# Kernel tuning notes

Measured on AMD Instinct MI355X. Metric: run time of the kernel, lower is better.

## Reference

```python
import jax, jax.numpy as jnp
import numpy as np

_NORM12 = np.array([[3,1,1,1,3,3,3,3],[1,3,1,1,3,3,3,3],[1,1,3,1,3,3,3,3],[1,1,1,3,3,3,3,3],[3,3,3,1,3,3,1,1],[3,3,3,1,3,1,3,1],[3,3,3,1,1,3,3,1],[3,3,3,1,3,1,1,3],[3,3,3,1,1,3,1,3],[3,3,3,1,1,1,3,3],[3,3,1,3,3,3,1,1],[3,3,1,3,3,1,3,1],[3,3,1,3,1,3,3,1],[3,3,1,3,3,1,1,3],[3,3,1,3,1,3,1,3],[3,3,1,3,1,1,3,3],[3,1,3,3,3,3,1,1],[3,1,3,3,3,1,3,1],[3,1,3,3,1,3,3,1],[3,1,3,3,3,1,1,3],[3,1,3,3,1,3,1,3],[1,3,3,3,1,1,3,3],[1,3,3,3,3,3,1,1],[1,3,3,3,3,1,3,1],[1,3,3,3,1,3,3,1],[1,3,3,3,3,1,1,3],[1,3,3,3,1,3,1,3],[1,1,3,3,1,3,3,3],[3,3,1,1,3,3,3,1]], dtype=np.float32) / 2.0


def _build_tables():
    # abs_grid: nonneg half-integer D8+1/2 abs patterns with norm^2 <= 10 (227 rows,
    # lexicographically sorted like torch.unique(dim=0)), plus 29 norm-12 extras -> 256 rows.
    vals = np.arange(4, dtype=np.float32) + 0.5  # {0.5,1.5,2.5,3.5}
    mesh = np.stack(np.meshgrid(*([vals] * 8), indexing='ij'), axis=-1).reshape(-1, 8)
    d8abs = mesh[(mesh ** 2).sum(-1) <= 10.0]
    d8abs = np.unique(d8abs, axis=0)
    abs_grid = np.concatenate([d8abs, _NORM12], axis=0)  # [256, 8]
    grid_abs_odd = (np.round(abs_grid.sum(-1)).astype(np.int64) % 2) == 1
    # grid_part = E8 lattice points (even # of sign flips of abs rows, last coord
    # pre-negated for odd-sum rows) filtered to: at most one of the first 7 coords < 0
    # and min(first 7) >= -0.5. This equals _E8P_GRID[_PARITY_IDX] + 0.25 after filtering.
    ap = abs_grid.copy()
    ap[:, 7] *= np.where(grid_abs_odd, -1.0, 1.0).astype(np.float32)
    bits = (np.arange(256)[:, None] >> np.arange(8)[None, :]) & 1
    signs = (1.0 - 2.0 * bits[(bits.sum(-1) % 2) == 0]).astype(np.float32)  # [128, 8]
    pts = (ap[:, None, :] * signs[None, :, :]).reshape(-1, 8)
    keep = ((pts[:, :7] < 0).sum(-1) <= 1) & (pts[:, :7].min(-1) >= -0.5)
    grid_part = pts[keep]
    grid_part_norm = (grid_part ** 2).sum(-1)
    # part_abs_map: nearest abs_grid row of |grid_part| (exact match; same argmax form as torch)
    scores = 2.0 * np.abs(grid_part) @ abs_grid.T - (abs_grid ** 2).sum(-1)
    part_abs_map = scores.argmax(-1).astype(np.int32)
    return grid_part, grid_part_norm, part_abs_map, grid_abs_odd


def setup_inputs() -> dict:
    gp, gpn, pam, gao = _build_tables()
    key = jax.random.key(0)
    X = jax.random.normal(key, (131072, 8), dtype=jnp.float32)
    return {
        'X': X,
        'grid_part': jnp.asarray(gp, dtype=jnp.float32),
        'grid_part_norm': jnp.asarray(gpn, dtype=jnp.float32),
        'part_abs_map': jnp.asarray(pam, dtype=jnp.int32),
        'grid_abs_odd': jnp.asarray(gao),
        'bit_map': jnp.asarray(2 ** np.arange(8), dtype=jnp.int32),
    }


_PERM = jnp.array([0, 2, 4, 6, 1, 3, 5, 7])


def _fast_quantize_part(X, grid_part, grid_part_norm, part_abs_map, grid_abs_odd, bit_map, parity):
    Xa = jnp.abs(X)
    neg = X < 0
    odd_row = (neg.sum(-1) % 2) == 1                       # [m]
    flip = (jnp.arange(8) == 7)[None, :] & odd_row[:, None]  # negate col 7 for odd rows
    X_part = jnp.where(flip, -Xa, Xa)
    mask = 1.0 - 2.0 * neg.astype(X.dtype)
    mask = jnp.where(flip, -mask, mask)
    scores = 2.0 * (X_part @ grid_part.T) - grid_part_norm  # [m, G]
    Xqidx = jnp.argmax(scores, axis=-1)
    roundout = grid_part[Xqidx]                            # [m, 8]
    vals = roundout * mask
    err = jnp.sqrt(jnp.sum((X - vals) ** 2, axis=-1))
    abs_idx = part_abs_map[Xqidx].astype(jnp.int32)
    sign_mask = ((roundout < 0) ^ (mask < 0))[:, _PERM]
    sign_mask = sign_mask.at[:, 7].set(sign_mask[:, 7] ^ grid_abs_odd[abs_idx])
    sign_mask = sign_mask.at[:, 0].set(sign_mask[:, 0] ^ parity)
    mask_idx = jnp.sum(sign_mask.astype(jnp.int32) * bit_map, axis=-1)
    idx = (abs_idx << 8) + mask_idx
    return vals, idx, err


def reference(X, grid_part, grid_part_norm, part_abs_map, grid_abs_odd, bit_map):
    quarter = jnp.asarray(0.25, X.dtype)
    pv, pi, pe = _fast_quantize_part(X + quarter, grid_part, grid_part_norm, part_abs_map, grid_abs_odd, bit_map, True)
    mv, mi, me = _fast_quantize_part(X - quarter, grid_part, grid_part_norm, part_abs_map, grid_abs_odd, bit_map, False)
    which = pe < me
    final_vals = jnp.where(which[:, None], pv - quarter, mv + quarter)
    final_idx = jnp.where(which, pi, mi)
    return final_vals, final_idx
```

## Files before the change

kernel.cpp:

```cpp
#include <hip/hip_runtime.h>
#include <math.h>

#define NT   256
#define ROWS 128
#define NW   4
#define MAXA 320

typedef _Float16 h8 __attribute__((ext_vector_type(8)));

static __device__ __forceinline__ unsigned f16_ru(float v) {
    _Float16 h = (_Float16)v;
    unsigned short b;
    __builtin_memcpy(&b, &h, 2);
    if ((float)h < v) b = (b & 0x8000) ? (unsigned short)(b - 1) : (unsigned short)(b + 1);
    return (unsigned)b;
}
static __device__ __forceinline__ float f16_lo(unsigned bits) {
    unsigned short s = (unsigned short)(bits & 0xffffu);
    _Float16 h;
    __builtin_memcpy(&h, &s, 2);
    return (float)h;
}

__global__ __launch_bounds__(NT, 4)
void e8p_quant_kernel(const float* __restrict__ X,
                      const float* __restrict__ gp,
                      const float* __restrict__ gn,
                      const int* __restrict__ pam,
                      float* __restrict__ out,
                      int N, int G)
{
#pragma clang fp contract(off)
    __shared__ h8             labs[MAXA];
    __shared__ unsigned short lmeta[MAXA];
    __shared__ unsigned short lj0[MAXA];
    __shared__ float    cb_bb[2][NW][ROWS];
    __shared__ float    cb_ev[2][NW][ROWS];
    __shared__ unsigned cb_h [2][NW][ROWS];
    __shared__ unsigned cb_ij[2][NW][ROWS];

    const int NG = pam[G - 1] + 1;

    const float4* gp4 = reinterpret_cast<const float4*>(gp);
    for (int j = threadIdx.x; j < G; j += NT) {
        int a = pam[j];
        bool st = (j == 0) || (pam[j - 1] != a);
        if (st) {
            float4 A = gp4[2 * j], B = gp4[2 * j + 1];
            float gv[8] = {A.x, A.y, A.z, A.w, B.x, B.y, B.z, B.w};
            h8 h;
#pragma unroll
            for (int k = 0; k < 8; ++k) h[k] = (_Float16)gv[k];
            labs[a] = h;
            int hm = 0;
#pragma unroll
            for (int k = 0; k < 7; ++k) hm |= int(fabsf(gv[k]) == 0.5f) << k;
            int nc = (int)((gn[j] - 2.0f) * 4.0f + 0.5f);
            lmeta[a] = (unsigned short)(hm | (nc << 8));
            lj0[a] = (unsigned short)j;
        }
    }
    __syncthreads();

    const int lane = threadIdx.x & 63;
    const int w    = threadIdx.x >> 6;
    const int rb   = blockIdx.x * ROWS;

    float xf[2][8], xp[2][8], xm[2][8];
    int msbp[2], msbm[2], oddp[2], oddm[2];
    float DLT[2];
    const float4* x4 = reinterpret_cast<const float4*>(X);
#pragma unroll
    for (int rr = 0; rr < 2; ++rr) {
        int r = rb + lane + (rr << 6);
        int rc = (r < N) ? r : (N - 1);
        float4 a0 = x4[2 * rc], a1 = x4[2 * rc + 1];
        float xr[8] = {a0.x, a0.y, a0.z, a0.w, a1.x, a1.y, a1.z, a1.w};
        int nbp = 0, nbm = 0; float Sp = 0.f, Sm = 0.f;
#pragma unroll
        for (int k = 0; k < 8; ++k) {
            xf[rr][k] = xr[k];
            float sp = xr[k] + 0.25f, sm = xr[k] - 0.25f;
            nbp |= int(sp < 0.f) << k;  nbm |= int(sm < 0.f) << k;
            xp[rr][k] = fabsf(sp);  xm[rr][k] = fabsf(sm);
            Sp += xp[rr][k]; Sm += xm[rr][k];
        }
        int op = __popc(nbp) & 1, om = __popc(nbm) & 1;
        if (op) xp[rr][7] = -xp[rr][7];
        if (om) xm[rr][7] = -xm[rr][7];
        oddp[rr] = op; oddm[rr] = om;
        msbp[rr] = nbp ^ (op << 7);  msbm[rr] = nbm ^ (om << 7);
        DLT[rr] = fmaf(3.5f * fmaxf(Sp, Sm), 3.0e-6f, 2.5e-5f);
    }

    float bt[2][2], ev[2][2], s0v[2][2], s1v[2][2];
    int   i0[2][2], i1[2][2];
#pragma unroll
    for (int rr = 0; rr < 2; ++rr)
#pragma unroll
        for (int pp = 0; pp < 2; ++pp) {
            bt[rr][pp] = -3.0e38f; ev[rr][pp] = -3.0e38f;
            s0v[rr][pp] = -3.0e38f; s1v[rr][pp] = -3.0e38f;
            i0[rr][pp] = 0; i1[rr][pp] = 0;
        }

    const int Q = (NG + NW - 1) / NW;
    const int abeg = w * Q, aend = min(NG, abeg + Q);

    for (int a = abeg; a < aend; ++a) {
        h8 hv = labs[a];
        int meta = __builtin_amdgcn_readfirstlane((int)lmeta[a]);
        int hm = meta & 0x7f;
        float nnh = fmaf(-0.125f, (float)(meta >> 8), -1.0f);
        float g0=(float)hv[0], g1=(float)hv[1], g2=(float)hv[2], g3=(float)hv[3];
        float g4=(float)hv[4], g5=(float)hv[5], g6=(float)hv[6], g7=(float)hv[7];
        float m2c7 = -2.0f * g7;

        float sc[2][2], wv[2][2], rm[2][2];
#pragma unroll
        for (int rr = 0; rr < 2; ++rr) {
            float s = fmaf(xp[rr][0], g0, nnh);
            s = fmaf(xp[rr][1], g1, s); s = fmaf(xp[rr][2], g2, s);
            s = fmaf(xp[rr][3], g3, s); s = fmaf(xp[rr][4], g4, s);
            s = fmaf(xp[rr][5], g5, s); s = fmaf(xp[rr][6], g6, s);
            s = fmaf(xp[rr][7], g7, s);
            sc[rr][0] = s;
            float t = fmaf(xm[rr][0], g0, nnh);
            t = fmaf(xm[rr][1], g1, t); t = fmaf(xm[rr][2], g2, t);
            t = fmaf(xm[rr][3], g3, t); t = fmaf(xm[rr][4], g4, t);
            t = fmaf(xm[rr][5], g5, t); t = fmaf(xm[rr][6], g6, t);
            t = fmaf(xm[rr][7], g7, t);
            sc[rr][1] = t;
            wv[rr][0] = fmaf(m2c7, xp[rr][7], s);
            wv[rr][1] = fmaf(m2c7, xm[rr][7], t);
            rm[rr][0] = s; rm[rr][1] = t;
        }
#pragma unroll
        for (int i = 0; i < 7; ++i) {
            if (hm & (1 << i)) {
                rm[0][0] = fmaxf(rm[0][0], wv[0][0] - xp[0][i]);
                rm[0][1] = fmaxf(rm[0][1], wv[0][1] - xm[0][i]);
                rm[1][0] = fmaxf(rm[1][0], wv[1][0] - xp[1][i]);
                rm[1][1] = fmaxf(rm[1][1], wv[1][1] - xm[1][i]);
            }
        }
#pragma unroll
        for (int rr = 0; rr < 2; ++rr)
#pragma unroll
            for (int pp = 0; pp < 2; ++pp) {
                float v = rm[rr][pp];
                if (v >= bt[rr][pp]) {
                    ev[rr][pp] = fmaxf(ev[rr][pp], s1v[rr][pp]);
                    s1v[rr][pp] = s0v[rr][pp]; i1[rr][pp] = i0[rr][pp];
                    s0v[rr][pp] = v;           i0[rr][pp] = a;
                    bt[rr][pp] = fmaxf(bt[rr][pp], v - DLT[rr]);
                }
            }
    }

#pragma unroll
    for (int rr = 0; rr < 2; ++rr) {
        int rowL = lane + (rr << 6);
#pragma unroll
        for (int pp = 0; pp < 2; ++pp) {
            cb_bb[pp][w][rowL] = fmaxf(s0v[rr][pp], fmaxf(s1v[rr][pp], ev[rr][pp]));
            cb_ev[pp][w][rowL] = ev[rr][pp];
            cb_h [pp][w][rowL] = f16_ru(s0v[rr][pp]) | (f16_ru(s1v[rr][pp]) << 16);
            cb_ij[pp][w][rowL] = (unsigned)i0[rr][pp] | ((unsigned)i1[rr][pp] << 16);
        }
    }
    __syncthreads();

    const int t = threadIdx.x;
    if (t >= ROWS) return;
    const int row = rb + t;
    if (row >= N) return;
    const int rs = (t >= 64) ? 1 : 0;

    double xpd[8], xmd[8];
#pragma unroll
    for (int k = 0; k < 8; ++k) {
        double xd = (double)xf[rs][k];
        xpd[k] = fabs(xd + 0.25);
        xmd[k] = fabs(xd - 0.25);
    }
    if (oddp[rs]) xpd[7] = -xpd[7];
    if (oddm[rs]) xmd[7] = -xmd[7];

    auto evalRow = [&](int a, const double* xd, double& bd, int& brow, int& bflip) {
        h8 hv = labs[a];
        int meta = (int)lmeta[a];
        int hm = meta & 0x7f;
        double nd = 2.0 + 0.25 * (double)(meta >> 8);
        double a0=(double)(float)hv[0], a1=(double)(float)hv[1];
        double a2=(double)(float)hv[2], a3=(double)(float)hv[3];
        double a4=(double)(float)hv[4], a5=(double)(float)hv[5];
        double a6=(double)(float)hv[6], a7=(double)(float)hv[7];
        double s = xd[0] * a0;
        s = fma(xd[1], a1, s); s = fma(xd[2], a2, s); s = fma(xd[3], a3, s);
        s = fma(xd[4], a4, s); s = fma(xd[5], a5, s); s = fma(xd[6], a6, s);
        s = fma(xd[7], a7, s);
        double sc0 = fma(2.0, s, -nd);
        if (sc0 > bd) { bd = sc0; brow = a; bflip = -1; }
        double sb2 = sc0 - 4.0 * (xd[7] * a7);
#pragma unroll
        for (int i = 0; i < 7; ++i) {
            if (hm & (1 << i)) {
                double sv = sb2 - 2.0 * xd[i];
                if (sv > bd) { bd = sv; brow = a; bflip = i; }
            }
        }
    };

    auto resolve = [&](int pp, const double* xd, int& browO, int& bflipO) {
        float B = fmaxf(fmaxf(cb_bb[pp][0][t], cb_bb[pp][1][t]),
                        fmaxf(cb_bb[pp][2][t], cb_bb[pp][3][t]));
        float thr = B - DLT[rs];
        bool ok = (cb_ev[pp][0][t] < thr) && (cb_ev[pp][1][t] < thr) &&
                  (cb_ev[pp][2][t] < thr) && (cb_ev[pp][3][t] < thr);
        double bd = -1.0e300; int brow = 0, bflip = -1;
        if (ok) {
#pragma unroll
            for (int w2 = 0; w2 < NW; ++w2) {
                unsigned hh = cb_h[pp][w2][t], ij = cb_ij[pp][w2][t];
                if (f16_lo(hh >> 16) >= thr) evalRow((int)(ij >> 16), xd, bd, brow, bflip);
                if (f16_lo(hh & 0xffffu) >= thr) evalRow((int)(ij & 0xffffu), xd, bd, brow, bflip);
            }
        } else {
            for (int a = 0; a < NG; ++a) evalRow(a, xd, bd, brow, bflip);
        }
        browO = brow; bflipO = bflip;
    };

    int prow, pflip, mrow, mflip;
    resolve(0, xpd, prow, pflip);
    resolve(1, xmd, mrow, mflip);

    double vp[8], vm[8];
    double errP, errM; int idxP, idxM;
    auto finish = [&](int brow, int bflip, double sgn_quarter, int msb, int par,
                      double* v, double& errO, int& idxO) {
#pragma clang fp contract(off)
        h8 hv = labs[brow];
        float g[8];
#pragma unroll
        for (int k = 0; k < 8; ++k) g[k] = (float)hv[k];
        if (bflip >= 0) {
#pragma unroll
            for (int k = 0; k < 7; ++k) if (bflip == k) g[k] = -g[k];
            g[7] = -g[7];
        }
        int gneg = 0; float sumabs = 0.0f;
#pragma unroll
        for (int k = 0; k < 8; ++k) {
            gneg |= int(g[k] < 0.0f) << k;
            sumabs += fabsf(g[k]);
        }
        double vv[8];
#pragma unroll
        for (int k = 0; k < 8; ++k) {
            unsigned u = __float_as_uint(g[k]) ^ ((((unsigned)msb >> k) & 1u) << 31);
            double val = (double)__uint_as_float(u);
            vv[k] = val;
            v[k] = val;
        }
        double d[8];
#pragma unroll
        for (int k = 0; k < 8; ++k) {
            double xs = (double)xf[rs][k] + sgn_quarter;
            d[k] = xs - vv[k];
        }
        double q0 = d[0]*d[0], q1 = d[1]*d[1], q2 = d[2]*d[2], q3 = d[3]*d[3];
        double q4 = d[4]*d[4], q5 = d[5]*d[5], q6 = d[6]*d[6], q7 = d[7]*d[7];
        double e = ((q0 + q1) + (q2 + q3)) + ((q4 + q5) + (q6 + q7));
        errO = sqrt(e);
        int godd = ((int)(sumabs + 0.5f)) & 1;
        int sb = gneg ^ msb;
        int mi = (((sb >> 0) & 1) ^ par)
               | (((sb >> 2) & 1) << 1)
               | (((sb >> 4) & 1) << 2)
               | (((sb >> 6) & 1) << 3)
               | (((sb >> 1) & 1) << 4)
               | (((sb >> 3) & 1) << 5)
               | (((sb >> 5) & 1) << 6)
               | ((((sb >> 7) & 1) ^ godd) << 7);
        idxO = (brow << 8) + mi;
    };

    finish(prow, pflip, +0.25, msbp[rs], 1, vp, errP, idxP);
    finish(mrow, mflip, -0.25, msbm[rs], 0, vm, errM, idxM);
    bool which = errP < errM;

    float ov[8];
#pragma unroll
    for (int k = 0; k < 8; ++k) {
        double o = which ? (vp[k] - 0.25) : (vm[k] + 0.25);
        ov[k] = (float)o;
    }
    float4* o4 = reinterpret_cast<float4*>(out + (size_t)row * 8);
    o4[0] = make_float4(ov[0], ov[1], ov[2], ov[3]);
    o4[1] = make_float4(ov[4], ov[5], ov[6], ov[7]);
    out[(size_t)N * 8 + row] = (float)(which ? idxP : idxM);
}

extern "C" void kernel_launch(void* const* d_in, const int* in_sizes, int n_in,
                              void* d_out, int out_size, void* d_ws, size_t ws_size,
                              hipStream_t stream)
{
    const float* X   = (const float*)d_in[0];
    const float* gp  = (const float*)d_in[1];
    const float* gn  = (const float*)d_in[2];
    const int*   pam = (const int*)d_in[3];
    float* out = (float*)d_out;

    int N = in_sizes[0] / 8;
    int G = in_sizes[1] / 8;
    int blocks = (N + ROWS - 1) / ROWS;
    e8p_quant_kernel<<<blocks, NT, 0, stream>>>(X, gp, gn, pam, out, N, G);
}
```

Measured before the change: 74.62 us.

## Pack plus/minus scores into float2 FMA and branchless top-2 update

The plus- and minus-shift vectors are packed as float2 pairs so the scoring dot products and corrections can map to packed FP32 instructions (v_pk_fma_f32 on CDNA). The per-coordinate max of (wv - x_i) is rewritten as wv minus the min over masked coordinates, which cuts the number of max operations. The top-2 candidate update becomes branchless selects, and the loop is unrolled by 2. An unused shared array is also dropped. The min-based rewrite changes floating-point rounding slightly relative to the per-term max, which could shift near-tie decisions.

New measurement: 99.86 us. 1.34x slower.

```diff
diff --git a/kernel.cpp b/kernel.cpp
--- a/kernel.cpp
+++ b/kernel.cpp
@@ -7,6 +7,7 @@
 #define MAXA 320
 
 typedef _Float16 h8 __attribute__((ext_vector_type(8)));
+typedef float    v2f __attribute__((ext_vector_type(2)));
 
 static __device__ __forceinline__ unsigned f16_ru(float v) {
     _Float16 h = (_Float16)v;
@@ -33,7 +34,6 @@
 #pragma clang fp contract(off)
     __shared__ h8             labs[MAXA];
     __shared__ unsigned short lmeta[MAXA];
-    __shared__ unsigned short lj0[MAXA];
     __shared__ float    cb_bb[2][NW][ROWS];
     __shared__ float    cb_ev[2][NW][ROWS];
     __shared__ unsigned cb_h [2][NW][ROWS];
@@ -57,7 +57,6 @@
             for (int k = 0; k < 7; ++k) hm |= int(fabsf(gv[k]) == 0.5f) << k;
             int nc = (int)((gn[j] - 2.0f) * 4.0f + 0.5f);
             lmeta[a] = (unsigned short)(hm | (nc << 8));
-            lj0[a] = (unsigned short)j;
         }
     }
     __syncthreads();
@@ -66,7 +65,8 @@
     const int w    = threadIdx.x >> 6;
     const int rb   = blockIdx.x * ROWS;
 
-    float xf[2][8], xp[2][8], xm[2][8];
+    float xf[2][8];
+    v2f   xv[2][8];
     int msbp[2], msbm[2], oddp[2], oddm[2];
     float DLT[2];
     const float4* x4 = reinterpret_cast<const float4*>(X);
@@ -77,20 +77,23 @@
         float4 a0 = x4[2 * rc], a1 = x4[2 * rc + 1];
         float xr[8] = {a0.x, a0.y, a0.z, a0.w, a1.x, a1.y, a1.z, a1.w};
         int nbp = 0, nbm = 0; float Sp = 0.f, Sm = 0.f;
+        float xpf[8], xmf[8];
 #pragma unroll
         for (int k = 0; k < 8; ++k) {
             xf[rr][k] = xr[k];
             float sp = xr[k] + 0.25f, sm = xr[k] - 0.25f;
             nbp |= int(sp < 0.f) << k;  nbm |= int(sm < 0.f) << k;
-            xp[rr][k] = fabsf(sp);  xm[rr][k] = fabsf(sm);
-            Sp += xp[rr][k]; Sm += xm[rr][k];
+            xpf[k] = fabsf(sp);  xmf[k] = fabsf(sm);
+            Sp += xpf[k]; Sm += xmf[k];
         }
         int op = __popc(nbp) & 1, om = __popc(nbm) & 1;
-        if (op) xp[rr][7] = -xp[rr][7];
-        if (om) xm[rr][7] = -xm[rr][7];
+        if (op) xpf[7] = -xpf[7];
+        if (om) xmf[7] = -xmf[7];
         oddp[rr] = op; oddm[rr] = om;
         msbp[rr] = nbp ^ (op << 7);  msbm[rr] = nbm ^ (om << 7);
         DLT[rr] = fmaf(3.5f * fmaxf(Sp, Sm), 3.0e-6f, 2.5e-5f);
+#pragma unroll
+        for (int k = 0; k < 8; ++k) xv[rr][k] = (v2f){xpf[k], xmf[k]};
     }
 
     float bt[2][2], ev[2][2], s0v[2][2], s1v[2][2];
@@ -107,6 +110,7 @@
     const int Q = (NG + NW - 1) / NW;
     const int abeg = w * Q, aend = min(NG, abeg + Q);
 
+#pragma unroll 2
     for (int a = abeg; a < aend; ++a) {
         h8 hv = labs[a];
         int meta = __builtin_amdgcn_readfirstlane((int)lmeta[a]);
@@ -115,46 +119,45 @@
         float g0=(float)hv[0], g1=(float)hv[1], g2=(float)hv[2], g3=(float)hv[3];
         float g4=(float)hv[4], g5=(float)hv[5], g6=(float)hv[6], g7=(float)hv[7];
         float m2c7 = -2.0f * g7;
-
-        float sc[2][2], wv[2][2], rm[2][2];
+        v2f nn2 = {nnh, nnh};
+        v2f c72 = {m2c7, m2c7};
+
+        v2f rmv[2];
 #pragma unroll
         for (int rr = 0; rr < 2; ++rr) {
-            float s = fmaf(xp[rr][0], g0, nnh);
-            s = fmaf(xp[rr][1], g1, s); s = fmaf(xp[rr][2], g2, s);
-            s = fmaf(xp[rr][3], g3, s); s = fmaf(xp[rr][4], g4, s);
-            s = fmaf(xp[rr][5], g5, s); s = fmaf(xp[rr][6], g6, s);
-            s = fmaf(xp[rr][7], g7, s);
-            sc[rr][0] = s;
-            float t = fmaf(xm[rr][0], g0, nnh);
-            t = fmaf(xm[rr][1], g1, t); t = fmaf(xm[rr][2], g2, t);
-            t = fmaf(xm[rr][3], g3, t); t = fmaf(xm[rr][4], g4, t);
-            t = fmaf(xm[rr][5], g5, t); t = fmaf(xm[rr][6], g6, t);
-            t = fmaf(xm[rr][7], g7, t);
-            sc[rr][1] = t;
-            wv[rr][0] = fmaf(m2c7, xp[rr][7], s);
-            wv[rr][1] = fmaf(m2c7, xm[rr][7], t);
-            rm[rr][0] = s; rm[rr][1] = t;
-        }
-#pragma unroll
-        for (int i = 0; i < 7; ++i) {
-            if (hm & (1 << i)) {
-                rm[0][0] = fmaxf(rm[0][0], wv[0][0] - xp[0][i]);
-                rm[0][1] = fmaxf(rm[0][1], wv[0][1] - xm[0][i]);
-                rm[1][0] = fmaxf(rm[1][0], wv[1][0] - xp[1][i]);
-                rm[1][1] = fmaxf(rm[1][1], wv[1][1] - xm[1][i]);
-            }
+            v2f acc = __builtin_elementwise_fma(xv[rr][0], (v2f){g0, g0}, nn2);
+            acc = __builtin_elementwise_fma(xv[rr][1], (v2f){g1, g1}, acc);
+            acc = __builtin_elementwise_fma(xv[rr][2], (v2f){g2, g2}, acc);
+            acc = __builtin_elementwise_fma(xv[rr][3], (v2f){g3, g3}, acc);
+            acc = __builtin_elementwise_fma(xv[rr][4], (v2f){g4, g4}, acc);
+            acc = __builtin_elementwise_fma(xv[rr][5], (v2f){g5, g5}, acc);
+            acc = __builtin_elementwise_fma(xv[rr][6], (v2f){g6, g6}, acc);
+            acc = __builtin_elementwise_fma(xv[rr][7], (v2f){g7, g7}, acc);
+            v2f wv = __builtin_elementwise_fma(c72, xv[rr][7], acc);
+            v2f mn = {1.0e30f, 1.0e30f};
+            if (hm & 1)   mn = __builtin_elementwise_min(mn, xv[rr][0]);
+            if (hm & 2)   mn = __builtin_elementwise_min(mn, xv[rr][1]);
+            if (hm & 4)   mn = __builtin_elementwise_min(mn, xv[rr][2]);
+            if (hm & 8)   mn = __builtin_elementwise_min(mn, xv[rr][3]);
+            if (hm & 16)  mn = __builtin_elementwise_min(mn, xv[rr][4]);
+            if (hm & 32)  mn = __builtin_elementwise_min(mn, xv[rr][5]);
+            if (hm & 64)  mn = __builtin_elementwise_min(mn, xv[rr][6]);
+            rmv[rr] = __builtin_elementwise_max(acc, wv - mn);
         }
 #pragma unroll
         for (int rr = 0; rr < 2; ++rr)
 #pragma unroll
             for (int pp = 0; pp < 2; ++pp) {
-                float v = rm[rr][pp];
-                if (v >= bt[rr][pp]) {
-                    ev[rr][pp] = fmaxf(ev[rr][pp], s1v[rr][pp]);
-                    s1v[rr][pp] = s0v[rr][pp]; i1[rr][pp] = i0[rr][pp];
-                    s0v[rr][pp] = v;           i0[rr][pp] = a;
-                    bt[rr][pp] = fmaxf(bt[rr][pp], v - DLT[rr]);
-                }
+                float v = (pp == 0) ? rmv[rr].x : rmv[rr].y;
+                bool c = v >= bt[rr][pp];
+                float evn = fmaxf(ev[rr][pp], s1v[rr][pp]);
+                float btn = fmaxf(bt[rr][pp], v - DLT[rr]);
+                ev[rr][pp]  = c ? evn        : ev[rr][pp];
+                s1v[rr][pp] = c ? s0v[rr][pp] : s1v[rr][pp];
+                i1[rr][pp]  = c ? i0[rr][pp]  : i1[rr][pp];
+                s0v[rr][pp] = c ? v           : s0v[rr][pp];
+                i0[rr][pp]  = c ? a           : i0[rr][pp];
+                bt[rr][pp]  = c ? btn         : bt[rr][pp];
             }
     }
 
```

## Split candidate scan over 8 waves and track branchless top-2 per wave

Applied to the files above, without the earlier changes.

Doubles the block to 512 threads so the abs-row scan is divided across 8 waves instead of 4, halving each wave's loop length. The per-row top-2/eviction bookkeeping becomes a branchless best/second-best max-min update with a single index. The flip refinement is recomputed as one min over the flagged coordinates instead of a per-coordinate max chain. The resolve step keeps only the best candidate per wave, so its exact fallback over all rows fires whenever any wave's second-best is within tolerance. The cost is more waves per block, a longer shared-memory reduction in resolve, and more frequent full double-precision rescans.

Measured after the change: 183.6 us. 2.46x slower.

```diff
diff --git a/kernel.cpp b/kernel.cpp
--- a/kernel.cpp
+++ b/kernel.cpp
@@ -1,28 +1,14 @@
 #include <hip/hip_runtime.h>
 #include <math.h>
 
-#define NT   256
+#define NT   512
 #define ROWS 128
-#define NW   4
+#define NW   8
 #define MAXA 320
 
 typedef _Float16 h8 __attribute__((ext_vector_type(8)));
 
-static __device__ __forceinline__ unsigned f16_ru(float v) {
-    _Float16 h = (_Float16)v;
-    unsigned short b;
-    __builtin_memcpy(&b, &h, 2);
-    if ((float)h < v) b = (b & 0x8000) ? (unsigned short)(b - 1) : (unsigned short)(b + 1);
-    return (unsigned)b;
-}
-static __device__ __forceinline__ float f16_lo(unsigned bits) {
-    unsigned short s = (unsigned short)(bits & 0xffffu);
-    _Float16 h;
-    __builtin_memcpy(&h, &s, 2);
-    return (float)h;
-}
-
-__global__ __launch_bounds__(NT, 4)
+__global__ __launch_bounds__(NT, 6)
 void e8p_quant_kernel(const float* __restrict__ X,
                       const float* __restrict__ gp,
                       const float* __restrict__ gn,
@@ -33,11 +19,9 @@
 #pragma clang fp contract(off)
     __shared__ h8             labs[MAXA];
     __shared__ unsigned short lmeta[MAXA];
-    __shared__ unsigned short lj0[MAXA];
-    __shared__ float    cb_bb[2][NW][ROWS];
-    __shared__ float    cb_ev[2][NW][ROWS];
-    __shared__ unsigned cb_h [2][NW][ROWS];
-    __shared__ unsigned cb_ij[2][NW][ROWS];
+    __shared__ float          cb_b1[2][NW][ROWS];
+    __shared__ float          cb_b2[2][NW][ROWS];
+    __shared__ unsigned short cb_id[2][NW][ROWS];
 
     const int NG = pam[G - 1] + 1;
 
@@ -57,7 +41,6 @@
             for (int k = 0; k < 7; ++k) hm |= int(fabsf(gv[k]) == 0.5f) << k;
             int nc = (int)((gn[j] - 2.0f) * 4.0f + 0.5f);
             lmeta[a] = (unsigned short)(hm | (nc << 8));
-            lj0[a] = (unsigned short)j;
         }
     }
     __syncthreads();
@@ -93,15 +76,13 @@
         DLT[rr] = fmaf(3.5f * fmaxf(Sp, Sm), 3.0e-6f, 2.5e-5f);
     }
 
-    float bt[2][2], ev[2][2], s0v[2][2], s1v[2][2];
-    int   i0[2][2], i1[2][2];
+    float b1[2][2], b2[2][2];
+    int   ia[2][2];
 #pragma unroll
     for (int rr = 0; rr < 2; ++rr)
 #pragma unroll
         for (int pp = 0; pp < 2; ++pp) {
-            bt[rr][pp] = -3.0e38f; ev[rr][pp] = -3.0e38f;
-            s0v[rr][pp] = -3.0e38f; s1v[rr][pp] = -3.0e38f;
-            i0[rr][pp] = 0; i1[rr][pp] = 0;
+            b1[rr][pp] = -3.0e38f; b2[rr][pp] = -3.0e38f; ia[rr][pp] = 0;
         }
 
     const int Q = (NG + NW - 1) / NW;
@@ -116,46 +97,76 @@
         float g4=(float)hv[4], g5=(float)hv[5], g6=(float)hv[6], g7=(float)hv[7];
         float m2c7 = -2.0f * g7;
 
-        float sc[2][2], wv[2][2], rm[2][2];
-#pragma unroll
-        for (int rr = 0; rr < 2; ++rr) {
-            float s = fmaf(xp[rr][0], g0, nnh);
-            s = fmaf(xp[rr][1], g1, s); s = fmaf(xp[rr][2], g2, s);
-            s = fmaf(xp[rr][3], g3, s); s = fmaf(xp[rr][4], g4, s);
-            s = fmaf(xp[rr][5], g5, s); s = fmaf(xp[rr][6], g6, s);
-            s = fmaf(xp[rr][7], g7, s);
-            sc[rr][0] = s;
-            float t = fmaf(xm[rr][0], g0, nnh);
-            t = fmaf(xm[rr][1], g1, t); t = fmaf(xm[rr][2], g2, t);
-            t = fmaf(xm[rr][3], g3, t); t = fmaf(xm[rr][4], g4, t);
-            t = fmaf(xm[rr][5], g5, t); t = fmaf(xm[rr][6], g6, t);
-            t = fmaf(xm[rr][7], g7, t);
-            sc[rr][1] = t;
-            wv[rr][0] = fmaf(m2c7, xp[rr][7], s);
-            wv[rr][1] = fmaf(m2c7, xm[rr][7], t);
-            rm[rr][0] = s; rm[rr][1] = t;
-        }
+        float s00, s01, s10, s11;
+        {
+            float s = fmaf(xp[0][0], g0, nnh);
+            s = fmaf(xp[0][1], g1, s); s = fmaf(xp[0][2], g2, s);
+            s = fmaf(xp[0][3], g3, s); s = fmaf(xp[0][4], g4, s);
+            s = fmaf(xp[0][5], g5, s); s = fmaf(xp[0][6], g6, s);
+            s = fmaf(xp[0][7], g7, s);
+            s00 = s;
+            float t = fmaf(xm[0][0], g0, nnh);
+            t = fmaf(xm[0][1], g1, t); t = fmaf(xm[0][2], g2, t);
+            t = fmaf(xm[0][3], g3, t); t = fmaf(xm[0][4], g4, t);
+            t = fmaf(xm[0][5], g5, t); t = fmaf(xm[0][6], g6, t);
+            t = fmaf(xm[0][7], g7, t);
+            s01 = t;
+        }
+        {
+            float s = fmaf(xp[1][0], g0, nnh);
+            s = fmaf(xp[1][1], g1, s); s = fmaf(xp[1][2], g2, s);
+            s = fmaf(xp[1][3], g3, s); s = fmaf(xp[1][4], g4, s);
+            s = fmaf(xp[1][5], g5, s); s = fmaf(xp[1][6], g6, s);
+            s = fmaf(xp[1][7], g7, s);
+            s10 = s;
+            float t = fmaf(xm[1][0], g0, nnh);
+            t = fmaf(xm[1][1], g1, t); t = fmaf(xm[1][2], g2, t);
+            t = fmaf(xm[1][3], g3, t); t = fmaf(xm[1][4], g4, t);
+            t = fmaf(xm[1][5], g5, t); t = fmaf(xm[1][6], g6, t);
+            t = fmaf(xm[1][7], g7, t);
+            s11 = t;
+        }
+        float wv00 = fmaf(m2c7, xp[0][7], s00);
+        float wv01 = fmaf(m2c7, xm[0][7], s01);
+        float wv10 = fmaf(m2c7, xp[1][7], s10);
+        float wv11 = fmaf(m2c7, xm[1][7], s11);
+        float mn00 = 1.0e30f, mn01 = 1.0e30f, mn10 = 1.0e30f, mn11 = 1.0e30f;
 #pragma unroll
         for (int i = 0; i < 7; ++i) {
             if (hm & (1 << i)) {
-                rm[0][0] = fmaxf(rm[0][0], wv[0][0] - xp[0][i]);
-                rm[0][1] = fmaxf(rm[0][1], wv[0][1] - xm[0][i]);
-                rm[1][0] = fmaxf(rm[1][0], wv[1][0] - xp[1][i]);
-                rm[1][1] = fmaxf(rm[1][1], wv[1][1] - xm[1][i]);
+                mn00 = fminf(mn00, xp[0][i]); mn01 = fminf(mn01, xm[0][i]);
+                mn10 = fminf(mn10, xp[1][i]); mn11 = fminf(mn11, xm[1][i]);
             }
         }
-#pragma unroll
-        for (int rr = 0; rr < 2; ++rr)
-#pragma unroll
-            for (int pp = 0; pp < 2; ++pp) {
-                float v = rm[rr][pp];
-                if (v >= bt[rr][pp]) {
-                    ev[rr][pp] = fmaxf(ev[rr][pp], s1v[rr][pp]);
-                    s1v[rr][pp] = s0v[rr][pp]; i1[rr][pp] = i0[rr][pp];
-                    s0v[rr][pp] = v;           i0[rr][pp] = a;
-                    bt[rr][pp] = fmaxf(bt[rr][pp], v - DLT[rr]);
-                }
-            }
+        float rm00 = fmaxf(s00, wv00 - mn00);
+        float rm01 = fmaxf(s01, wv01 - mn01);
+        float rm10 = fmaxf(s10, wv10 - mn10);
+        float rm11 = fmaxf(s11, wv11 - mn11);
+
+        {
+            bool c = rm00 > b1[0][0];
+            ia[0][0] = c ? a : ia[0][0];
+            b2[0][0] = fmaxf(b2[0][0], fminf(rm00, b1[0][0]));
+            b1[0][0] = fmaxf(b1[0][0], rm00);
+        }
+        {
+            bool c = rm01 > b1[0][1];
+            ia[0][1] = c ? a : ia[0][1];
+            b2[0][1] = fmaxf(b2[0][1], fminf(rm01, b1[0][1]));
+            b1[0][1] = fmaxf(b1[0][1], rm01);
+        }
+        {
+            bool c = rm10 > b1[1][0];
+            ia[1][0] = c ? a : ia[1][0];
+            b2[1][0] = fmaxf(b2[1][0], fminf(rm10, b1[1][0]));
+            b1[1][0] = fmaxf(b1[1][0], rm10);
+        }
+        {
+            bool c = rm11 > b1[1][1];
+            ia[1][1] = c ? a : ia[1][1];
+            b2[1][1] = fmaxf(b2[1][1], fminf(rm11, b1[1][1]));
+            b1[1][1] = fmaxf(b1[1][1], rm11);
+        }
     }
 
 #pragma unroll
@@ -163,10 +174,9 @@
         int rowL = lane + (rr << 6);
 #pragma unroll
         for (int pp = 0; pp < 2; ++pp) {
-            cb_bb[pp][w][rowL] = fmaxf(s0v[rr][pp], fmaxf(s1v[rr][pp], ev[rr][pp]));
-            cb_ev[pp][w][rowL] = ev[rr][pp];
-            cb_h [pp][w][rowL] = f16_ru(s0v[rr][pp]) | (f16_ru(s1v[rr][pp]) << 16);
-            cb_ij[pp][w][rowL] = (unsigned)i0[rr][pp] | ((unsigned)i1[rr][pp] << 16);
+            cb_b1[pp][w][rowL] = b1[rr][pp];
+            cb_b2[pp][w][rowL] = b2[rr][pp];
+            cb_id[pp][w][rowL] = (unsigned short)ia[rr][pp];
         }
     }
     __syncthreads();
@@ -213,18 +223,19 @@
     };
 
     auto resolve = [&](int pp, const double* xd, int& browO, int& bflipO) {
-        float B = fmaxf(fmaxf(cb_bb[pp][0][t], cb_bb[pp][1][t]),
-                        fmaxf(cb_bb[pp][2][t], cb_bb[pp][3][t]));
+        float B = cb_b1[pp][0][t];
+#pragma unroll
+        for (int w2 = 1; w2 < NW; ++w2) B = fmaxf(B, cb_b1[pp][w2][t]);
         float thr = B - DLT[rs];
-        bool ok = (cb_ev[pp][0][t] < thr) && (cb_ev[pp][1][t] < thr) &&
-                  (cb_ev[pp][2][t] < thr) && (cb_ev[pp][3][t] < thr);
+        bool ok = true;
+#pragma unroll
+        for (int w2 = 0; w2 < NW; ++w2) ok = ok && (cb_b2[pp][w2][t] < thr);
         double bd = -1.0e300; int brow = 0, bflip = -1;
         if (ok) {
 #pragma unroll
             for (int w2 = 0; w2 < NW; ++w2) {
-                unsigned hh = cb_h[pp][w2][t], ij = cb_ij[pp][w2][t];
-                if (f16_lo(hh >> 16) >= thr) evalRow((int)(ij >> 16), xd, bd, brow, bflip);
-                if (f16_lo(hh & 0xffffu) >= thr) evalRow((int)(ij & 0xffffu), xd, bd, brow, bflip);
+                if (cb_b1[pp][w2][t] >= thr)
+                    evalRow((int)cb_id[pp][w2][t], xd, bd, brow, bflip);
             }
         } else {
             for (int a = 0; a < NG; ++a) evalRow(a, xd, bd, brow, bflip);
```
